# Optimization experiments

Hardware: AMD Instinct MI355X
Metric: run time of the kernel (lower is better)

The kernel has to match this reference:

```python
import jax, jax.numpy as jnp
import numpy as np

FILTER_FACTOR = 10  # init kwarg


def median_filter2d(x, k, padding="REFLECT", constant_values=0.0):
    """Faithful port of tfa.image.median_filter2d for NHWC float input.

    tfa pads with pad_top=(k-1)//2, pad_bottom=k-1-pad_top (same for width),
    extracts k*k patches per pixel/channel, and takes the element that
    tf.nn.top_k(patches, area//2+1)[..., -1] yields, i.e. the value at
    ascending-sorted index (area-1)//2.
    """
    B, H, W, C = x.shape
    pt = (k - 1) // 2
    pb = k - 1 - pt
    mode = {"REFLECT": "reflect", "SYMMETRIC": "symmetric", "CONSTANT": "constant"}[padding]
    if mode == "constant":
        xp = jnp.pad(x, ((0, 0), (pt, pb), (pt, pb), (0, 0)), mode=mode,
                     constant_values=constant_values)
    else:
        xp = jnp.pad(x, ((0, 0), (pt, pb), (pt, pb), (0, 0)), mode=mode)
    # Gather sliding windows via advanced indexing (vectorized, no data loops).
    ih = jnp.arange(H)[:, None] + jnp.arange(k)[None, :]  # (H, k)
    iw = jnp.arange(W)[:, None] + jnp.arange(k)[None, :]  # (W, k)
    rows = xp[:, ih]                 # (B, H, k, Wp, C)
    patches = rows[:, :, :, iw]      # (B, H, k, W, k, C)
    patches = patches.transpose(0, 1, 3, 5, 2, 4).reshape(B, H, W, C, k * k)
    area = k * k
    med = jnp.sort(patches, axis=-1)[..., (area - 1) // 2]  # (B, H, W, C)
    return med


def setup_inputs() -> dict:
    key = jax.random.key(0)
    k1, k2 = jax.random.split(key)
    inputs = jax.random.uniform(k1, (2, 224, 224, 3), dtype=jnp.float32)
    # layer draws blend ~ U[0.1, 1.0)
    blend = jax.random.uniform(k2, (1,), dtype=jnp.float32) * 0.9 + 0.1
    return {"inputs": inputs, "blend": blend}


def reference(inputs, blend):
    # training=True path: median filter then tfa.image.blend(filtered, inputs, blend)
    # blend(image1, image2, f) = image1 + f * (image2 - image1)
    k = inputs.shape[1] // FILTER_FACTOR  # height // filter_factor
    filt = median_filter2d(inputs, k, padding="REFLECT", constant_values=0.0)
    f = blend[0]
    return filt + f * (inputs - filt)
```

## Files before the change

kernel.cpp:

```cpp
#include <hip/hip_runtime.h>


#define HH 224
#define WW 224
#define CHN 3
#define KK 22
#define PT 10
#define AREA (KK * KK)
#define RANK 242
#define PXW 8
#define XGS (WW / PXW)
#define DT 2

#define INFF  __int_as_float(0x7f800000)
#define NINFF __int_as_float(0xff800000)

__device__ __forceinline__ int reflect224(int g) {
    int a = abs(g);
    return min(a, 2 * (HH - 1) - a);
}

__device__ __forceinline__ int count8(const float v[8], float t) {
    int c = 0;
#pragma unroll
    for (int i = 0; i < 8; ++i)
        c += __popcll(__ballot(v[i] < t));
    return c;
}

__device__ __forceinline__ void gather(float v[8], const float* __restrict__ img,
                                       const int voff[8], int lane, int x) {
    if (x >= PT && x <= WW - 1 - (KK - 1 - PT)) {
        const float* base = img + (x - PT) * CHN;
#pragma unroll
        for (int i = 0; i < 8; ++i) v[i] = base[voff[i]];
    } else {
#pragma unroll
        for (int i = 0; i < 8; ++i) {
            int s   = i * 64 + lane;
            int se  = min(s, AREA - 1);
            int row = se / KK;
            int col = se - row * KK;
            int gy672 = voff[i] - col * CHN;
            int gx = reflect224(x - PT + col);
            v[i] = img[gy672 + gx * CHN];
        }
    }
    v[7] = (lane < AREA - 448) ? v[7] : INFF;
}

__global__ __launch_bounds__(256)
void median_blend_kernel(const float* __restrict__ in,
                         const float* __restrict__ blend,
                         float* __restrict__ out) {
    const int lane = threadIdx.x & 63;
    const int wid  = threadIdx.x >> 6;
    const int wg = blockIdx.x * 4 + wid;
    const int xg = wg % XGS;
    const int t1 = wg / XGS;
    const int y  = t1 % HH;
    const int t2 = t1 / HH;
    const int c  = t2 % CHN;
    const int b  = t2 / CHN;

    const float f = blend[0];
    const float* img  = in  + (size_t)b * (HH * WW * CHN) + c;
    float*       outp = out + (size_t)b * (HH * WW * CHN) + c;

    int voff[8];
#pragma unroll
    for (int i = 0; i < 8; ++i) {
        int s   = i * 64 + lane;
        int se  = min(s, AREA - 1);
        int row = se / KK;
        int col = se - row * KK;
        int gy  = reflect224(y - PT + row);
        voff[i] = gy * (WW * CHN) + col * CHN;
    }

    const int x0 = xg * PXW;
    float tprev = 0.5f;

#pragma unroll 1
    for (int j = 0; j < PXW; j += 2) {
        const int xA = x0 + j;
        const int xB = xA + 1;

        float vA[8], vB[8];
        gather(vA, img, voff, lane, xA);
        gather(vB, img, voff, lane, xB);

        float tA = tprev, tB = tprev;
        int CA = count8(vA, tA);
        int CB = count8(vB, tB);
        float loA = 0.0f, hiA = 1.0f, loB = 0.0f, hiB = 1.0f;
        int cloA = 0, chiA = AREA, cloB = 0, chiB = AREA;
        bool actA = true, actB = true;
#pragma unroll 1
        for (int it = 0; it < 16 && (actA || actB); ++it) {
            if (actA) {
                int d = CA - RANK;
                if (d >= -DT && d <= DT) actA = false;
                else {
                    if (d > 0) { hiA = tA; chiA = CA; }
                    else       { loA = tA; cloA = CA; }
                    float tn = loA + (hiA - loA) * (float)(RANK - cloA) *
                               __builtin_amdgcn_rcpf((float)(chiA - cloA));
                    if (!(tn > loA && tn < hiA)) {
                        tn = 0.5f * (loA + hiA);
                        if (!(tn > loA && tn < hiA)) actA = false;
                    }
                    if (actA) { tA = tn; CA = count8(vA, tA); }
                }
            }
            if (actB) {
                int d = CB - RANK;
                if (d >= -DT && d <= DT) actB = false;
                else {
                    if (d > 0) { hiB = tB; chiB = CB; }
                    else       { loB = tB; cloB = CB; }
                    float tn = loB + (hiB - loB) * (float)(RANK - cloB) *
                               __builtin_amdgcn_rcpf((float)(chiB - cloB));
                    if (!(tn > loB && tn < hiB)) {
                        tn = 0.5f * (loB + hiB);
                        if (!(tn > loB && tn < hiB)) actB = false;
                    }
                    if (actB) { tB = tn; CB = count8(vB, tB); }
                }
            }
        }

        const int dA = CA - RANK, dB = CB - RANK;
        const bool topA = (dA >= 0), topB = (dB >= 0);
        int eA = topA ? dA + 1 : -dA;
        int eB = topB ? dB + 1 : -dB;
        const int sgnA = topA ? 0 : 0x80000000;
        const int sgnB = topB ? 0 : 0x80000000;
#pragma unroll
        for (int i = 0; i < 8; ++i) {
            bool ltA = vA[i] < tA;
            float sA = __int_as_float(__float_as_int(vA[i]) ^ sgnA);
            vA[i] = (ltA == topA) ? sA : NINFF;
            bool ltB = vB[i] < tB;
            float sB = __int_as_float(__float_as_int(vB[i]) ^ sgnB);
            vB[i] = (ltB == topB) ? sB : NINFF;
        }

        float medA = tA, medB = tB;
        bool doneA = false, doneB = false;
#pragma unroll 1
        for (int r = 0; r < 300 && !(doneA && doneB); ++r) {
            float mA = fmaxf(fmaxf(fmaxf(vA[0], vA[1]), fmaxf(vA[2], vA[3])),
                             fmaxf(fmaxf(vA[4], vA[5]), fmaxf(vA[6], vA[7])));
            float mB = fmaxf(fmaxf(fmaxf(vB[0], vB[1]), fmaxf(vB[2], vB[3])),
                             fmaxf(fmaxf(vB[4], vB[5]), fmaxf(vB[6], vB[7])));
#pragma unroll
            for (int off = 32; off > 0; off >>= 1) {
                mA = fmaxf(mA, __shfl_xor(mA, off, 64));
                mB = fmaxf(mB, __shfl_xor(mB, off, 64));
            }
            if (!doneA) {
                int q = 0;
#pragma unroll
                for (int i = 0; i < 8; ++i)
                    q += __popcll(__ballot(vA[i] == mA));
                if (eA <= q) {
                    medA = __int_as_float(__float_as_int(mA) ^ sgnA);
                    doneA = true;
                } else {
                    eA -= q;
#pragma unroll
                    for (int i = 0; i < 8; ++i)
                        vA[i] = (vA[i] == mA) ? NINFF : vA[i];
                }
            }
            if (!doneB) {
                int q = 0;
#pragma unroll
                for (int i = 0; i < 8; ++i)
                    q += __popcll(__ballot(vB[i] == mB));
                if (eB <= q) {
                    medB = __int_as_float(__float_as_int(mB) ^ sgnB);
                    doneB = true;
                } else {
                    eB -= q;
#pragma unroll
                    for (int i = 0; i < 8; ++i)
                        vB[i] = (vB[i] == mB) ? NINFF : vB[i];
                }
            }
        }
        tprev = medB;

        const float xcA = img[y * (WW * CHN) + xA * CHN];
        const float xcB = img[y * (WW * CHN) + xB * CHN];
        if (lane == 0) {
            outp[y * (WW * CHN) + xA * CHN] = medA + f * (xcA - medA);
            outp[y * (WW * CHN) + xB * CHN] = medB + f * (xcB - medB);
        }
    }
}

extern "C" void kernel_launch(void* const* d_in, const int* in_sizes, int n_in,
                              void* d_out, int out_size, void* d_ws, size_t ws_size,
                              hipStream_t stream) {
    const float* in    = (const float*)d_in[0];
    const float* blend = (const float*)d_in[1];
    float* out = (float*)d_out;

    const int nwaves  = 2 * CHN * HH * XGS;
    const int nblocks = nwaves / 4;
    median_blend_kernel<<<nblocks, 256, 0, stream>>>(in, blend, out);
}
```

Baseline: 163.7 us.

## Refine median threshold to exact rank and fuse final max reduction

The threshold search now iterates until the count below the threshold equals the rank exactly. It uses a cheaper secant step that assumes a uniform value density (d/AREA) in place of the reciprocal-based interpolation. When both pixels hit the exact rank, the median is the max of the values below the threshold. The two pixels' max reductions are packed into one wave reduction using ds_swizzle/bpermute instead of a shfl_xor chain. The peel loop becomes a fallback only. The cost is possibly more search iterations, and the density assumption suits the uniform test inputs.

```diff
diff --git a/kernel.cpp b/kernel.cpp
--- a/kernel.cpp
+++ b/kernel.cpp
@@ -10,7 +10,6 @@
 #define RANK 242
 #define PXW 8
 #define XGS (WW / PXW)
-#define DT 2
 
 #define INFF  __int_as_float(0x7f800000)
 #define NINFF __int_as_float(0xff800000)
@@ -26,6 +25,59 @@
     for (int i = 0; i < 8; ++i)
         c += __popcll(__ballot(v[i] < t));
     return c;
+}
+
+__device__ __forceinline__ float half_bfly(float m) {
+    m = fmaxf(m, __int_as_float(__builtin_amdgcn_ds_swizzle(__float_as_int(m), 0x401F)));
+    m = fmaxf(m, __int_as_float(__builtin_amdgcn_ds_swizzle(__float_as_int(m), 0x201F)));
+    m = fmaxf(m, __int_as_float(__builtin_amdgcn_ds_swizzle(__float_as_int(m), 0x101F)));
+    m = fmaxf(m, __int_as_float(__builtin_amdgcn_ds_swizzle(__float_as_int(m), 0x081F)));
+    m = fmaxf(m, __int_as_float(__builtin_amdgcn_ds_swizzle(__float_as_int(m), 0x041F)));
+    return m;
+}
+
+__device__ __forceinline__ float foldtree(const float v[8], float t, float ninf) {
+    float s[8];
+#pragma unroll
+    for (int i = 0; i < 8; ++i)
+        s[i] = (v[i] < t) ? v[i] : ninf;
+    return fmaxf(fmaxf(fmaxf(s[0], s[1]), fmaxf(s[2], s[3])),
+                 fmaxf(fmaxf(s[4], s[5]), fmaxf(s[6], s[7])));
+}
+
+__device__ __forceinline__ float wavemax(float s, int axor32) {
+    s = fmaxf(s, __int_as_float(
+            __builtin_amdgcn_ds_bpermute(axor32, __float_as_int(s))));
+    return half_bfly(s);
+}
+
+__device__ __forceinline__ float peel1(float v[8], float t, int d, int axor32) {
+    const bool top = (d >= 0);
+    int e = top ? d + 1 : -d;
+    const int sgn = top ? 0 : (int)0x80000000;
+#pragma unroll
+    for (int i = 0; i < 8; ++i) {
+        bool lt = v[i] < t;
+        float s = __int_as_float(__float_as_int(v[i]) ^ sgn);
+        v[i] = (lt == top) ? s : NINFF;
+    }
+    float med = t;
+#pragma unroll 1
+    for (int r = 0; r < 300; ++r) {
+        float m = fmaxf(fmaxf(fmaxf(v[0], v[1]), fmaxf(v[2], v[3])),
+                        fmaxf(fmaxf(v[4], v[5]), fmaxf(v[6], v[7])));
+        m = wavemax(m, axor32);
+        int q = 0;
+#pragma unroll
+        for (int i = 0; i < 8; ++i)
+            q += __popcll(__ballot(v[i] == m));
+        if (e <= q) { med = __int_as_float(__float_as_int(m) ^ sgn); break; }
+        e -= q;
+#pragma unroll
+        for (int i = 0; i < 8; ++i)
+            v[i] = (v[i] == m) ? NINFF : v[i];
+    }
+    return med;
 }
 
 __device__ __forceinline__ void gather(float v[8], const float* __restrict__ img,
@@ -78,6 +130,10 @@
         voff[i] = gy * (WW * CHN) + col * CHN;
     }
 
+    const int axor32 = (lane ^ 32) << 2;
+    const float ninf = NINFF;
+    const float NINV = -1.0f / (float)AREA;
+
     const int x0 = xg * PXW;
     float tprev = 0.5f;
 
@@ -93,110 +149,63 @@
         float tA = tprev, tB = tprev;
         int CA = count8(vA, tA);
         int CB = count8(vB, tB);
+        int dA = CA - RANK, dB = CB - RANK;
         float loA = 0.0f, hiA = 1.0f, loB = 0.0f, hiB = 1.0f;
-        int cloA = 0, chiA = AREA, cloB = 0, chiB = AREA;
-        bool actA = true, actB = true;
+        bool actA = (dA != 0), actB = (dB != 0);
 #pragma unroll 1
-        for (int it = 0; it < 16 && (actA || actB); ++it) {
+        for (int it = 0; it < 20 && (actA || actB); ++it) {
             if (actA) {
-                int d = CA - RANK;
-                if (d >= -DT && d <= DT) actA = false;
+                if (dA > 0) hiA = tA; else loA = tA;
+                float tn = fmaf((float)dA, NINV, tA);
+                if (!(tn > loA && tn < hiA)) tn = 0.5f * (loA + hiA);
+                if (!(tn > loA && tn < hiA)) actA = false;
                 else {
-                    if (d > 0) { hiA = tA; chiA = CA; }
-                    else       { loA = tA; cloA = CA; }
-                    float tn = loA + (hiA - loA) * (float)(RANK - cloA) *
-                               __builtin_amdgcn_rcpf((float)(chiA - cloA));
-                    if (!(tn > loA && tn < hiA)) {
-                        tn = 0.5f * (loA + hiA);
-                        if (!(tn > loA && tn < hiA)) actA = false;
-                    }
-                    if (actA) { tA = tn; CA = count8(vA, tA); }
+                    tA = tn;
+                    CA = count8(vA, tA);
+                    dA = CA - RANK;
+                    actA = (dA != 0);
                 }
             }
             if (actB) {
-                int d = CB - RANK;
-                if (d >= -DT && d <= DT) actB = false;
+                if (dB > 0) hiB = tB; else loB = tB;
+                float tn = fmaf((float)dB, NINV, tB);
+                if (!(tn > loB && tn < hiB)) tn = 0.5f * (loB + hiB);
+                if (!(tn > loB && tn < hiB)) actB = false;
                 else {
-                    if (d > 0) { hiB = tB; chiB = CB; }
-                    else       { loB = tB; cloB = CB; }
-                    float tn = loB + (hiB - loB) * (float)(RANK - cloB) *
-                               __builtin_amdgcn_rcpf((float)(chiB - cloB));
-                    if (!(tn > loB && tn < hiB)) {
-                        tn = 0.5f * (loB + hiB);
-                        if (!(tn > loB && tn < hiB)) actB = false;
-                    }
-                    if (actB) { tB = tn; CB = count8(vB, tB); }
+                    tB = tn;
+                    CB = count8(vB, tB);
+                    dB = CB - RANK;
+                    actB = (dB != 0);
                 }
             }
         }
 
-        const int dA = CA - RANK, dB = CB - RANK;
-        const bool topA = (dA >= 0), topB = (dB >= 0);
-        int eA = topA ? dA + 1 : -dA;
-        int eB = topB ? dB + 1 : -dB;
-        const int sgnA = topA ? 0 : 0x80000000;
-        const int sgnB = topB ? 0 : 0x80000000;
-#pragma unroll
-        for (int i = 0; i < 8; ++i) {
-            bool ltA = vA[i] < tA;
-            float sA = __int_as_float(__float_as_int(vA[i]) ^ sgnA);
-            vA[i] = (ltA == topA) ? sA : NINFF;
-            bool ltB = vB[i] < tB;
-            float sB = __int_as_float(__float_as_int(vB[i]) ^ sgnB);
-            vB[i] = (ltB == topB) ? sB : NINFF;
-        }
-
-        float medA = tA, medB = tB;
-        bool doneA = false, doneB = false;
-#pragma unroll 1
-        for (int r = 0; r < 300 && !(doneA && doneB); ++r) {
-            float mA = fmaxf(fmaxf(fmaxf(vA[0], vA[1]), fmaxf(vA[2], vA[3])),
-                             fmaxf(fmaxf(vA[4], vA[5]), fmaxf(vA[6], vA[7])));
-            float mB = fmaxf(fmaxf(fmaxf(vB[0], vB[1]), fmaxf(vB[2], vB[3])),
-                             fmaxf(fmaxf(vB[4], vB[5]), fmaxf(vB[6], vB[7])));
-#pragma unroll
-            for (int off = 32; off > 0; off >>= 1) {
-                mA = fmaxf(mA, __shfl_xor(mA, off, 64));
-                mB = fmaxf(mB, __shfl_xor(mB, off, 64));
-            }
-            if (!doneA) {
-                int q = 0;
-#pragma unroll
-                for (int i = 0; i < 8; ++i)
-                    q += __popcll(__ballot(vA[i] == mA));
-                if (eA <= q) {
-                    medA = __int_as_float(__float_as_int(mA) ^ sgnA);
-                    doneA = true;
-                } else {
-                    eA -= q;
-#pragma unroll
-                    for (int i = 0; i < 8; ++i)
-                        vA[i] = (vA[i] == mA) ? NINFF : vA[i];
-                }
-            }
-            if (!doneB) {
-                int q = 0;
-#pragma unroll
-                for (int i = 0; i < 8; ++i)
-                    q += __popcll(__ballot(vB[i] == mB));
-                if (eB <= q) {
-                    medB = __int_as_float(__float_as_int(mB) ^ sgnB);
-                    doneB = true;
-                } else {
-                    eB -= q;
-#pragma unroll
-                    for (int i = 0; i < 8; ++i)
-                        vB[i] = (vB[i] == mB) ? NINFF : vB[i];
-                }
-            }
-        }
-        tprev = medB;
+        float medA, medBall;
+        if (dA == 0 && dB == 0) {
+            float sA = foldtree(vA, tA, ninf);
+            float sB = foldtree(vB, tB, ninf);
+            sA = fmaxf(sA, __int_as_float(
+                    __builtin_amdgcn_ds_bpermute(axor32, __float_as_int(sA))));
+            sB = fmaxf(sB, __int_as_float(
+                    __builtin_amdgcn_ds_bpermute(axor32, __float_as_int(sB))));
+            float m = (lane < 32) ? sA : sB;
+            m = half_bfly(m);
+            medA = m;
+            medBall = __int_as_float(
+                __builtin_amdgcn_readlane(__float_as_int(m), 32));
+        } else {
+            medA = (dA == 0) ? wavemax(foldtree(vA, tA, ninf), axor32)
+                             : peel1(vA, tA, dA, axor32);
+            medBall = (dB == 0) ? wavemax(foldtree(vB, tB, ninf), axor32)
+                                : peel1(vB, tB, dB, axor32);
+        }
+        tprev = medBall;
 
         const float xcA = img[y * (WW * CHN) + xA * CHN];
         const float xcB = img[y * (WW * CHN) + xB * CHN];
         if (lane == 0) {
             outp[y * (WW * CHN) + xA * CHN] = medA + f * (xcA - medA);
-            outp[y * (WW * CHN) + xB * CHN] = medB + f * (xcB - medB);
+            outp[y * (WW * CHN) + xB * CHN] = medBall + f * (xcB - medBall);
         }
     }
 }
```

After: 194.7 us. +18.9%, slower.
